# Kernel optimization log

Hardware: AMD Instinct MI355X
Metric: run time of the kernel (lower is better)

## Reference

```python
import jax, jax.numpy as jnp
import numpy as np

LAYER_LAYOUT = [64, 128, 128, 128, 10]
B, D, D_OUT, L_GNN = 16, 128, 10, 3
N = sum(LAYER_LAYOUT)            # 458 nodes per graph


def _build_edge_index():
    # nn_to_edge_index: fully-connected bipartite edges between consecutive layers
    offs = np.cumsum([0] + LAYER_LAYOUT)
    src, dst = [], []
    for i in range(1, len(LAYER_LAYOUT)):
        s = np.arange(offs[i - 1], offs[i])
        d = np.arange(offs[i], offs[i + 1])
        ss, dd = np.meshgrid(s, d, indexing='ij')
        src.append(ss.ravel())
        dst.append(dd.ravel())
    return np.stack([np.concatenate(src), np.concatenate(dst)])  # [2, E]


def setup_inputs() -> dict:
    key = jax.random.key(0)
    ks = jax.random.split(key, 8)
    E = 42240
    edge_index = jnp.asarray(_build_edge_index(), dtype=jnp.int64)
    return {
        'node_features': jax.random.normal(ks[0], (B, N, D), jnp.float32),
        'edge_attr': jax.random.normal(ks[1], (B, E, D), jnp.float32),
        'w_msg': jax.random.normal(ks[2], (L_GNN, 3 * D, D), jnp.float32) / jnp.sqrt(3.0 * D),
        'b_msg': jnp.zeros((L_GNN, D), jnp.float32),
        'w_self': jax.random.normal(ks[3], (L_GNN, D, D), jnp.float32) / jnp.sqrt(1.0 * D),
        'b_self': jnp.zeros((L_GNN, D), jnp.float32),
        'w1': jax.random.normal(ks[4], (D, D), jnp.float32) / jnp.sqrt(1.0 * D),
        'b1': jnp.zeros((D,), jnp.float32),
        'w2': jax.random.normal(ks[5], (D, D), jnp.float32) / jnp.sqrt(1.0 * D),
        'b2': jnp.zeros((D,), jnp.float32),
        'w3': jax.random.normal(ks[6], (D, D_OUT), jnp.float32) / jnp.sqrt(1.0 * D),
        'b3': jnp.zeros((D_OUT,), jnp.float32),
        'edge_index': edge_index,
    }


def reference(node_features, edge_attr, w_msg, b_msg, w_self, b_self,
              w1, b1, w2, b2, w3, b3, edge_index):
    src, dst = edge_index[0], edge_index[1]
    E = src.shape[0]
    # in-degree per destination node (shared across the batch)
    deg = jax.ops.segment_sum(jnp.ones((E,), node_features.dtype), dst, num_segments=N)
    denom = jnp.maximum(deg, 1.0)[:, None]  # [N, 1]

    def aggregate(m):  # m: [B, E, D] -> [B, N, D] mean over incoming edges
        return jax.vmap(lambda mm: jax.ops.segment_sum(mm, dst, num_segments=N))(m) / denom

    x = node_features
    for l in range(L_GNN):
        # edge message: relu(W [x_src, x_dst, e])
        m = jnp.concatenate([x[:, src], x[:, dst], edge_attr], axis=-1)  # [B, E, 3D]
        m = jax.nn.relu(jnp.einsum('bef,fd->bed', m, w_msg[l]) + b_msg[l])
        agg = aggregate(m)  # [B, N, D]
        x = jax.nn.relu(jnp.einsum('bnf,fd->bnd', x, w_self[l]) + b_self[l] + agg)

    # graph_features == 'mean' over nodes, then proj_out MLP head
    g = x.mean(axis=1)  # [B, D]
    h = jax.nn.relu(g @ w1 + b1)
    h = jax.nn.relu(h @ w2 + b2)
    return h @ w3 + b3  # [B, D_OUT]
```

## Files before the change

### kernel.cpp

```cpp
#include <hip/hip_runtime.h>
#include <hip/hip_bf16.h>

#define D 128
#define NNODES 458
#define BATCH 16
#define ETOT 42240
#define LGNN 3
#define SPLITS 8

typedef __bf16 bf16x8 __attribute__((ext_vector_type(8)));
typedef float f32x4 __attribute__((ext_vector_type(4)));

__device__ inline bf16x8 cvt8v(f32x4 a, f32x4 b) {
    bf16x8 r;
    r[0] = (__bf16)a[0]; r[1] = (__bf16)a[1]; r[2] = (__bf16)a[2]; r[3] = (__bf16)a[3];
    r[4] = (__bf16)b[0]; r[5] = (__bf16)b[1]; r[6] = (__bf16)b[2]; r[7] = (__bf16)b[3];
    return r;
}

__global__ __launch_bounds__(256) void cvt_edge_kernel(
    const f32x4* __restrict__ src, bf16x8* __restrict__ dst)
{
    const size_t total = (size_t)BATCH * ETOT * (D / 8);
    size_t i = (size_t)blockIdx.x * 256 + threadIdx.x;
    const size_t stride = (size_t)gridDim.x * 256;
    for (; i < total; i += stride) {
        f32x4 a = __builtin_nontemporal_load(&src[2 * i]);
        f32x4 b = __builtin_nontemporal_load(&src[2 * i + 1]);
        dst[i] = cvt8v(a, b);
    }
}

__global__ __launch_bounds__(256) void node_proj_kernel(
    const float* __restrict__ x,
    const float* __restrict__ wmsg_l,
    const float* __restrict__ bmsg_l,
    const float* __restrict__ wself_l,
    const float* __restrict__ bself_l,
    float* __restrict__ asrc, float* __restrict__ bdst, float* __restrict__ xs,
    float* __restrict__ agg)
{
    const int b     = blockIdx.y;
    const int n0    = blockIdx.x * 16;
    const int which = blockIdx.z;
    const int tid   = threadIdx.x;

    __shared__ float xt[16 * D];
    for (int i = tid; i < 16 * D; i += 256) {
        int r = i >> 7;
        int n = n0 + r; if (n >= NNODES) n = NNODES - 1;
        xt[i] = x[((size_t)b * NNODES + n) * D + (i & 127)];
    }
    __syncthreads();

    const int d    = tid & 127;
    const int half = tid >> 7;

    const float* w = (which == 0) ? wmsg_l
                   : (which == 1) ? (wmsg_l + D * D)
                                  : wself_l;

    float acc[8] = {};
    for (int k = 0; k < D; ++k) {
        float wv = w[k * D + d];
#pragma unroll
        for (int r = 0; r < 8; ++r)
            acc[r] += xt[(half * 8 + r) * D + k] * wv;
    }

    const float bias = (which == 1) ? bmsg_l[d] : (which == 2) ? bself_l[d] : 0.f;
    float* outp = (which == 0) ? asrc : (which == 1) ? bdst : xs;
#pragma unroll
    for (int r = 0; r < 8; ++r) {
        int n = n0 + half * 8 + r;
        if (n < NNODES) {
            size_t o = ((size_t)b * NNODES + n) * D + d;
            outp[o] = acc[r] + bias;
            if (which == 0) agg[o] = 0.f;
        }
    }
}

__global__ __launch_bounds__(256) void edge_kernel(
    const bf16x8* __restrict__ eb,
    const float* __restrict__ w3,
    const float* __restrict__ asrc,
    const float* __restrict__ bdst,
    float* __restrict__ agg)
{
    const int tile  = blockIdx.x;
    const int b     = blockIdx.y;
    const int split = blockIdx.z;

    int j0, Nsrc, Ndst, e_off, src_off, dst_off;
    if (tile < 8)       { j0 = tile * 16;        Nsrc = 64;  Ndst = 128; e_off = 0;     src_off = 0;   dst_off = 64;  }
    else if (tile < 16) { j0 = (tile - 8) * 16;  Nsrc = 128; Ndst = 128; e_off = 8192;  src_off = 64;  dst_off = 192; }
    else if (tile < 24) { j0 = (tile - 16) * 16; Nsrc = 128; Ndst = 128; e_off = 24576; src_off = 192; dst_off = 320; }
    else                { j0 = 0;                Nsrc = 128; Ndst = 10;  e_off = 40960; src_off = 320; dst_off = 448; }

    const int chunk = Nsrc / SPLITS;
    const int s0    = split * chunk;

    const int tid  = threadIdx.x;
    const int wave = tid >> 6;
    const int lane = tid & 63;
    const int lm   = lane & 15;
    const int q    = lane >> 4;

    bf16x8 bfrag[2][4];
#pragma unroll
    for (int t = 0; t < 2; ++t) {
        int n = wave * 32 + t * 16 + lm;
#pragma unroll
        for (int kk = 0; kk < 4; ++kk)
#pragma unroll
            for (int j = 0; j < 8; ++j)
                bfrag[t][kk][j] = (__bf16)w3[(kk * 32 + q * 8 + j) * D + n];
    }

    float bpv[2][4];
#pragma unroll
    for (int t = 0; t < 2; ++t)
#pragma unroll
        for (int r = 0; r < 4; ++r) {
            int j = j0 + q * 4 + r; if (j > Ndst - 1) j = Ndst - 1;
            bpv[t][r] = bdst[((size_t)b * NNODES + dst_off + j) * D + wave * 32 + t * 16 + lm];
        }

    int m_eff = (j0 + lm < Ndst) ? lm : (Ndst - 1 - j0);
    const bf16x8* ap = eb +
        ((size_t)b * ETOT + e_off + (size_t)s0 * Ndst + j0 + m_eff) * 16 + q;
    const float* as_ptr = asrc + ((size_t)b * NNODES + src_off + s0) * D;

    float acc[2][4] = {};
#pragma unroll 4
    for (int s = 0; s < chunk; ++s) {
        bf16x8 afrag[4];
#pragma unroll
        for (int kk = 0; kk < 4; ++kk) afrag[kk] = ap[kk * 4];
        float as0 = as_ptr[wave * 32 + lm];
        float as1 = as_ptr[wave * 32 + 16 + lm];
        ap += Ndst * 16;
        as_ptr += D;

#pragma unroll
        for (int t = 0; t < 2; ++t) {
            f32x4 c = {0.f, 0.f, 0.f, 0.f};
#pragma unroll
            for (int kk = 0; kk < 4; ++kk)
                c = __builtin_amdgcn_mfma_f32_16x16x32_bf16(afrag[kk], bfrag[t][kk], c, 0, 0, 0);
            float as_d = t ? as1 : as0;
#pragma unroll
            for (int r = 0; r < 4; ++r) {
                float v = c[r] + as_d + bpv[t][r];
                acc[t][r] += fmaxf(v, 0.f);
            }
        }
    }

    const float inv_deg = 1.0f / (float)Nsrc;
#pragma unroll
    for (int t = 0; t < 2; ++t)
#pragma unroll
        for (int r = 0; r < 4; ++r) {
            int j = j0 + q * 4 + r;
            if (j < Ndst)
                atomicAdd(&agg[((size_t)b * NNODES + dst_off + j) * D + wave * 32 + t * 16 + lm],
                          acc[t][r] * inv_deg);
        }
}

__global__ __launch_bounds__(256) void update_kernel(
    const float4* __restrict__ xs, const float4* __restrict__ agg,
    float4* __restrict__ x)
{
    int i = blockIdx.x * 256 + threadIdx.x;
    int rowi = i >> 5;
    int n = rowi % NNODES;
    float4 v = xs[i];
    if (n >= 64) {
        float4 a = agg[i];
        v.x += a.x; v.y += a.y; v.z += a.z; v.w += a.w;
    }
    v.x = fmaxf(v.x, 0.f); v.y = fmaxf(v.y, 0.f);
    v.z = fmaxf(v.z, 0.f); v.w = fmaxf(v.w, 0.f);
    x[i] = v;
}

__global__ __launch_bounds__(256) void head_kernel(
    const float* __restrict__ x,
    const float* __restrict__ w1, const float* __restrict__ b1,
    const float* __restrict__ w2, const float* __restrict__ b2,
    const float* __restrict__ w3, const float* __restrict__ b3,
    float* __restrict__ out)
{
    const int b = blockIdx.x;
    const int tid = threadIdx.x;
    __shared__ float tmp[256];
    __shared__ float g[128], h1[128], h2[128];

    const int d = tid & 127, half = tid >> 7;
    float s = 0.f;
    for (int n = half; n < NNODES; n += 2)
        s += x[((size_t)b * NNODES + n) * D + d];
    tmp[tid] = s;
    __syncthreads();
    if (tid < 128) g[tid] = (tmp[tid] + tmp[tid + 128]) * (1.0f / (float)NNODES);
    __syncthreads();

    if (tid < 128) {
        float a = 0.f;
        for (int k = 0; k < D; ++k) a += g[k] * w1[k * D + tid];
        h1[tid] = fmaxf(a + b1[tid], 0.f);
    }
    __syncthreads();
    if (tid < 128) {
        float a = 0.f;
        for (int k = 0; k < D; ++k) a += h1[k] * w2[k * D + tid];
        h2[tid] = fmaxf(a + b2[tid], 0.f);
    }
    __syncthreads();
    if (tid < 10) {
        float a = 0.f;
        for (int k = 0; k < D; ++k) a += h2[k] * w3[k * 10 + tid];
        out[b * 10 + tid] = a + b3[tid];
    }
}

extern "C" void kernel_launch(void* const* d_in, const int* in_sizes, int n_in,
                              void* d_out, int out_size, void* d_ws, size_t ws_size,
                              hipStream_t stream) {
    const float* node_features = (const float*)d_in[0];
    const float* edge_attr     = (const float*)d_in[1];
    const float* w_msg         = (const float*)d_in[2];
    const float* b_msg         = (const float*)d_in[3];
    const float* w_self        = (const float*)d_in[4];
    const float* b_self        = (const float*)d_in[5];
    const float* w1 = (const float*)d_in[6];
    const float* b1 = (const float*)d_in[7];
    const float* w2 = (const float*)d_in[8];
    const float* b2 = (const float*)d_in[9];
    const float* w3 = (const float*)d_in[10];
    const float* b3 = (const float*)d_in[11];
    float* out = (float*)d_out;

    float* ws = (float*)d_ws;
    const size_t SZ = (size_t)BATCH * NNODES * D;
    float* x_ws = ws;
    float* asrc = ws + SZ;
    float* bdst = ws + 2 * SZ;
    float* xs   = ws + 3 * SZ;
    float* agg  = ws + 4 * SZ;
    bf16x8* eb  = (bf16x8*)(ws + 5 * SZ);

    cvt_edge_kernel<<<dim3(2048), 256, 0, stream>>>(
        (const f32x4*)edge_attr, eb);

    for (int l = 0; l < LGNN; ++l) {
        const float* xin    = (l == 0) ? node_features : x_ws;
        const float* wmsg_l = w_msg + (size_t)l * 384 * 128;
        node_proj_kernel<<<dim3(29, 16, 3), 256, 0, stream>>>(
            xin, wmsg_l, b_msg + l * 128, w_self + (size_t)l * 128 * 128,
            b_self + l * 128, asrc, bdst, xs, agg);
        edge_kernel<<<dim3(25, 16, SPLITS), 256, 0, stream>>>(
            eb, wmsg_l + 256 * 128, asrc, bdst, agg);
        update_kernel<<<dim3(916), 256, 0, stream>>>(
            (const float4*)xs, (const float4*)agg, (float4*)x_ws);
    }
    head_kernel<<<dim3(16), 256, 0, stream>>>(x_ws, w1, b1, w2, b2, w3, b3, out);
}
```

Measured before the change: 914.1 us.

## Fuse node update into projections, merge prep work, pre-transpose bf16 message weights

The per-layer update kernel is removed: the next layer's projection and the head kernel now apply relu(xs + agg) while loading. The three projection GEMMs (source, destination and self) are computed in one block, so the node tile is read once instead of three times. Edge conversion, a bf16 transpose of the edge-message weights and the layer-0 projection are merged into a single prep launch. The edge kernel can then load its weight fragments as vector bf16 reads instead of strided scalar float loads. This cuts launches and intermediate traffic, at the cost of more registers in the projection and xs/agg being updated in place.

```diff
diff --git a/kernel.cpp b/kernel.cpp
--- a/kernel.cpp
+++ b/kernel.cpp
@@ -18,72 +18,122 @@
     return r;
 }
 
-__global__ __launch_bounds__(256) void cvt_edge_kernel(
-    const f32x4* __restrict__ src, bf16x8* __restrict__ dst)
-{
-    const size_t total = (size_t)BATCH * ETOT * (D / 8);
-    size_t i = (size_t)blockIdx.x * 256 + threadIdx.x;
-    const size_t stride = (size_t)gridDim.x * 256;
-    for (; i < total; i += stride) {
-        f32x4 a = __builtin_nontemporal_load(&src[2 * i]);
-        f32x4 b = __builtin_nontemporal_load(&src[2 * i + 1]);
-        dst[i] = cvt8v(a, b);
-    }
-}
-
-__global__ __launch_bounds__(256) void node_proj_kernel(
-    const float* __restrict__ x,
-    const float* __restrict__ wmsg_l,
-    const float* __restrict__ bmsg_l,
-    const float* __restrict__ wself_l,
-    const float* __restrict__ bself_l,
-    float* __restrict__ asrc, float* __restrict__ bdst, float* __restrict__ xs,
-    float* __restrict__ agg)
-{
-    const int b     = blockIdx.y;
-    const int n0    = blockIdx.x * 16;
-    const int which = blockIdx.z;
-    const int tid   = threadIdx.x;
-
-    __shared__ float xt[16 * D];
-    for (int i = tid; i < 16 * D; i += 256) {
-        int r = i >> 7;
+__device__ __forceinline__ void proj_body(
+    int b, int n0, int mode,
+    const float* xsrc,
+    const float* aggin,
+    const float* __restrict__ wmsg_l, const float* __restrict__ bmsg_l,
+    const float* __restrict__ wself_l, const float* __restrict__ bself_l,
+    float* __restrict__ asrc, float* __restrict__ bdst,
+    float* xs_out, float* __restrict__ agg, float* xt)
+{
+    const int tid = threadIdx.x;
+    for (int i4 = tid; i4 < 512; i4 += 256) {
+        int r = i4 >> 5;
         int n = n0 + r; if (n >= NNODES) n = NNODES - 1;
-        xt[i] = x[((size_t)b * NNODES + n) * D + (i & 127)];
-    }
-    __syncthreads();
-
-    const int d    = tid & 127;
-    const int half = tid >> 7;
-
-    const float* w = (which == 0) ? wmsg_l
-                   : (which == 1) ? (wmsg_l + D * D)
-                                  : wself_l;
-
-    float acc[8] = {};
-    for (int k = 0; k < D; ++k) {
-        float wv = w[k * D + d];
-#pragma unroll
-        for (int r = 0; r < 8; ++r)
-            acc[r] += xt[(half * 8 + r) * D + k] * wv;
-    }
-
-    const float bias = (which == 1) ? bmsg_l[d] : (which == 2) ? bself_l[d] : 0.f;
-    float* outp = (which == 0) ? asrc : (which == 1) ? bdst : xs;
+        size_t o = ((size_t)b * NNODES + n) * 32 + (i4 & 31);
+        float4 v = ((const float4*)xsrc)[o];
+        if (mode) {
+            if (n >= 64) {
+                float4 a = ((const float4*)aggin)[o];
+                v.x += a.x; v.y += a.y; v.z += a.z; v.w += a.w;
+            }
+            v.x = fmaxf(v.x, 0.f); v.y = fmaxf(v.y, 0.f);
+            v.z = fmaxf(v.z, 0.f); v.w = fmaxf(v.w, 0.f);
+        }
+        ((float4*)xt)[i4] = v;
+    }
+    __syncthreads();
+
+    const int d = tid & 127, half = tid >> 7;
+    float acc0[8] = {}, acc1[8] = {}, acc2[8] = {};
+    const float4* xt4 = (const float4*)xt;
+    for (int k4 = 0; k4 < 32; ++k4) {
+        float4 xv[8];
+#pragma unroll
+        for (int r = 0; r < 8; ++r) xv[r] = xt4[(half * 8 + r) * 32 + k4];
+#pragma unroll
+        for (int i = 0; i < 4; ++i) {
+            int k = k4 * 4 + i;
+            float w1v = wmsg_l[k * D + d];
+            float w2v = wmsg_l[(D + k) * D + d];
+            float wsv = wself_l[k * D + d];
+#pragma unroll
+            for (int r = 0; r < 8; ++r) {
+                float xe = (i == 0) ? xv[r].x : (i == 1) ? xv[r].y
+                         : (i == 2) ? xv[r].z : xv[r].w;
+                acc0[r] += xe * w1v;
+                acc1[r] += xe * w2v;
+                acc2[r] += xe * wsv;
+            }
+        }
+    }
+    const float bm = bmsg_l[d], bs = bself_l[d];
 #pragma unroll
     for (int r = 0; r < 8; ++r) {
         int n = n0 + half * 8 + r;
         if (n < NNODES) {
             size_t o = ((size_t)b * NNODES + n) * D + d;
-            outp[o] = acc[r] + bias;
-            if (which == 0) agg[o] = 0.f;
-        }
-    }
+            asrc[o]   = acc0[r];
+            bdst[o]   = acc1[r] + bm;
+            xs_out[o] = acc2[r] + bs;
+            agg[o]    = 0.f;
+        }
+    }
+}
+
+__global__ __launch_bounds__(256) void prep_kernel(
+    const f32x4* __restrict__ edge_attr, bf16x8* __restrict__ eb,
+    const float* __restrict__ w_msg, __bf16* __restrict__ wT,
+    const float* __restrict__ node_features,
+    const float* __restrict__ bmsg0,
+    const float* __restrict__ wself0, const float* __restrict__ bself0,
+    float* __restrict__ asrc, float* __restrict__ bdst,
+    float* __restrict__ xs, float* __restrict__ agg)
+{
+    __shared__ float xt[16 * D];
+    const int bid = blockIdx.x;
+    const int tid = threadIdx.x;
+    if (bid < 2048) {
+        const size_t total = (size_t)BATCH * ETOT * (D / 8);
+        size_t i = (size_t)bid * 256 + tid;
+        const size_t stride = (size_t)2048 * 256;
+        for (; i < total; i += stride) {
+            f32x4 a = __builtin_nontemporal_load(&edge_attr[2 * i]);
+            f32x4 b = __builtin_nontemporal_load(&edge_attr[2 * i + 1]);
+            eb[i] = cvt8v(a, b);
+        }
+    } else if (bid < 2051) {
+        const int l = bid - 2048;
+        const float* w3s = w_msg + (size_t)l * 384 * 128 + 256 * 128;
+        __bf16* wTl = wT + (size_t)l * 128 * 128;
+        for (int idx = tid; idx < 128 * 128; idx += 256) {
+            int n = idx >> 7, k = idx & 127;
+            wTl[idx] = (__bf16)w3s[k * 128 + n];
+        }
+    } else {
+        const int bid2 = bid - 2051;
+        const int bx = bid2 % 29, b = bid2 / 29;
+        proj_body(b, bx * 16, 0, node_features, nullptr,
+                  w_msg, bmsg0, wself0, bself0, asrc, bdst, xs, agg, xt);
+    }
+}
+
+__global__ __launch_bounds__(256) void node_proj_kernel(
+    const float* xs_in, const float* __restrict__ agg_in,
+    const float* __restrict__ wmsg_l, const float* __restrict__ bmsg_l,
+    const float* __restrict__ wself_l, const float* __restrict__ bself_l,
+    float* __restrict__ asrc, float* __restrict__ bdst,
+    float* xs, float* __restrict__ agg)
+{
+    __shared__ float xt[16 * D];
+    proj_body(blockIdx.y, blockIdx.x * 16, 1, xs_in, agg_in,
+              wmsg_l, bmsg_l, wself_l, bself_l, asrc, bdst, xs, agg, xt);
 }
 
 __global__ __launch_bounds__(256) void edge_kernel(
     const bf16x8* __restrict__ eb,
-    const float* __restrict__ w3,
+    const __bf16* __restrict__ wT_l,
     const float* __restrict__ asrc,
     const float* __restrict__ bdst,
     float* __restrict__ agg)
@@ -113,9 +163,7 @@
         int n = wave * 32 + t * 16 + lm;
 #pragma unroll
         for (int kk = 0; kk < 4; ++kk)
-#pragma unroll
-            for (int j = 0; j < 8; ++j)
-                bfrag[t][kk][j] = (__bf16)w3[(kk * 32 + q * 8 + j) * D + n];
+            bfrag[t][kk] = *(const bf16x8*)(wT_l + n * 128 + kk * 32 + q * 8);
     }
 
     float bpv[2][4];
@@ -170,25 +218,8 @@
         }
 }
 
-__global__ __launch_bounds__(256) void update_kernel(
-    const float4* __restrict__ xs, const float4* __restrict__ agg,
-    float4* __restrict__ x)
-{
-    int i = blockIdx.x * 256 + threadIdx.x;
-    int rowi = i >> 5;
-    int n = rowi % NNODES;
-    float4 v = xs[i];
-    if (n >= 64) {
-        float4 a = agg[i];
-        v.x += a.x; v.y += a.y; v.z += a.z; v.w += a.w;
-    }
-    v.x = fmaxf(v.x, 0.f); v.y = fmaxf(v.y, 0.f);
-    v.z = fmaxf(v.z, 0.f); v.w = fmaxf(v.w, 0.f);
-    x[i] = v;
-}
-
 __global__ __launch_bounds__(256) void head_kernel(
-    const float* __restrict__ x,
+    const float* __restrict__ xs, const float* __restrict__ agg,
     const float* __restrict__ w1, const float* __restrict__ b1,
     const float* __restrict__ w2, const float* __restrict__ b2,
     const float* __restrict__ w3, const float* __restrict__ b3,
@@ -201,8 +232,12 @@
 
     const int d = tid & 127, half = tid >> 7;
     float s = 0.f;
-    for (int n = half; n < NNODES; n += 2)
-        s += x[((size_t)b * NNODES + n) * D + d];
+    for (int n = half; n < NNODES; n += 2) {
+        size_t o = ((size_t)b * NNODES + n) * D + d;
+        float v = xs[o];
+        if (n >= 64) v += agg[o];
+        s += fmaxf(v, 0.f);
+    }
     tmp[tid] = s;
     __syncthreads();
     if (tid < 128) g[tid] = (tmp[tid] + tmp[tid + 128]) * (1.0f / (float)NNODES);
@@ -246,26 +281,28 @@
 
     float* ws = (float*)d_ws;
     const size_t SZ = (size_t)BATCH * NNODES * D;
-    float* x_ws = ws;
-    float* asrc = ws + SZ;
-    float* bdst = ws + 2 * SZ;
-    float* xs   = ws + 3 * SZ;
-    float* agg  = ws + 4 * SZ;
-    bf16x8* eb  = (bf16x8*)(ws + 5 * SZ);
-
-    cvt_edge_kernel<<<dim3(2048), 256, 0, stream>>>(
-        (const f32x4*)edge_attr, eb);
+    float* asrc = ws;
+    float* bdst = ws + SZ;
+    float* xs   = ws + 2 * SZ;
+    float* agg  = ws + 3 * SZ;
+    bf16x8* eb  = (bf16x8*)(ws + 4 * SZ);
+    __bf16* wT  = (__bf16*)(ws + 4 * SZ + (size_t)BATCH * ETOT * (D / 2));
+
+    prep_kernel<<<dim3(2048 + 3 + 464), 256, 0, stream>>>(
+        (const f32x4*)edge_attr, eb, w_msg, wT, node_features,
+        b_msg, w_self, b_self, asrc, bdst, xs, agg);
 
     for (int l = 0; l < LGNN; ++l) {
-        const float* xin    = (l == 0) ? node_features : x_ws;
-        const float* wmsg_l = w_msg + (size_t)l * 384 * 128;
-        node_proj_kernel<<<dim3(29, 16, 3), 256, 0, stream>>>(
-            xin, wmsg_l, b_msg + l * 128, w_self + (size_t)l * 128 * 128,
-            b_self + l * 128, asrc, bdst, xs, agg);
+        if (l > 0) {
+            const float* wmsg_l = w_msg + (size_t)l * 384 * 128;
+            node_proj_kernel<<<dim3(29, 16), 256, 0, stream>>>(
+                xs, agg, wmsg_l, b_msg + l * 128,
+                w_self + (size_t)l * 128 * 128, b_self + l * 128,
+                asrc, bdst, xs, agg);
+        }
         edge_kernel<<<dim3(25, 16, SPLITS), 256, 0, stream>>>(
-            eb, wmsg_l + 256 * 128, asrc, bdst, agg);
-        update_kernel<<<dim3(916), 256, 0, stream>>>(
-            (const float4*)xs, (const float4*)agg, (float4*)x_ws);
-    }
-    head_kernel<<<dim3(16), 256, 0, stream>>>(x_ws, w1, b1, w2, b2, w3, b3, out);
-}
+            eb, wT + (size_t)l * 128 * 128, asrc, bdst, agg);
+    }
+    head_kernel<<<dim3(16), 256, 0, stream>>>(
+        xs, agg, w1, b1, w2, b2, w3, b3, out);
+}
```

New measurement: 3.105 ms. 3.4x slower.

## Replace edge-kernel atomics with two split partial buffers and pre-transposed bf16 weights

Applied to the files above, without the earlier changes.

The edge kernel's source dimension is now split into 2 chunks instead of 8. Each split writes its partial aggregate to its own buffer with plain stores rather than atomicAdd, so node_proj no longer zeroes agg. The update kernel sums the two partial buffers. A one-time kernel also transposes and converts the edge-message weight slice to bf16, so each block loads its B fragments with vector loads instead of 32 strided scalar loads. The trade-off is fewer blocks in the edge grid (800 instead of 3200) with a longer serial loop per block, plus one extra partial buffer to read in the update kernel.

```diff
diff --git a/kernel.cpp b/kernel.cpp
--- a/kernel.cpp
+++ b/kernel.cpp
@@ -6,7 +6,7 @@
 #define BATCH 16
 #define ETOT 42240
 #define LGNN 3
-#define SPLITS 8
+#define ESPLITS 2
 
 typedef __bf16 bf16x8 __attribute__((ext_vector_type(8)));
 typedef float f32x4 __attribute__((ext_vector_type(4)));
@@ -31,14 +31,25 @@
     }
 }
 
+__global__ __launch_bounds__(256) void wt_kernel(
+    const float* __restrict__ w_msg, __bf16* __restrict__ wT)
+{
+    const int l = blockIdx.x;
+    const float* w3s = w_msg + (size_t)l * 384 * 128 + 256 * 128;
+    __bf16* wTl = wT + (size_t)l * 128 * 128;
+    for (int idx = threadIdx.x; idx < 128 * 128; idx += 256) {
+        int n = idx >> 7, k = idx & 127;
+        wTl[idx] = (__bf16)w3s[k * 128 + n];
+    }
+}
+
 __global__ __launch_bounds__(256) void node_proj_kernel(
     const float* __restrict__ x,
     const float* __restrict__ wmsg_l,
     const float* __restrict__ bmsg_l,
     const float* __restrict__ wself_l,
     const float* __restrict__ bself_l,
-    float* __restrict__ asrc, float* __restrict__ bdst, float* __restrict__ xs,
-    float* __restrict__ agg)
+    float* __restrict__ asrc, float* __restrict__ bdst, float* __restrict__ xs)
 {
     const int b     = blockIdx.y;
     const int n0    = blockIdx.x * 16;
@@ -76,17 +87,16 @@
         if (n < NNODES) {
             size_t o = ((size_t)b * NNODES + n) * D + d;
             outp[o] = acc[r] + bias;
-            if (which == 0) agg[o] = 0.f;
         }
     }
 }
 
 __global__ __launch_bounds__(256) void edge_kernel(
     const bf16x8* __restrict__ eb,
-    const float* __restrict__ w3,
+    const __bf16* __restrict__ wT_l,
     const float* __restrict__ asrc,
     const float* __restrict__ bdst,
-    float* __restrict__ agg)
+    float* __restrict__ aggp)
 {
     const int tile  = blockIdx.x;
     const int b     = blockIdx.y;
@@ -98,7 +108,7 @@
     else if (tile < 24) { j0 = (tile - 16) * 16; Nsrc = 128; Ndst = 128; e_off = 24576; src_off = 192; dst_off = 320; }
     else                { j0 = 0;                Nsrc = 128; Ndst = 10;  e_off = 40960; src_off = 320; dst_off = 448; }
 
-    const int chunk = Nsrc / SPLITS;
+    const int chunk = Nsrc / ESPLITS;
     const int s0    = split * chunk;
 
     const int tid  = threadIdx.x;
@@ -113,9 +123,7 @@
         int n = wave * 32 + t * 16 + lm;
 #pragma unroll
         for (int kk = 0; kk < 4; ++kk)
-#pragma unroll
-            for (int j = 0; j < 8; ++j)
-                bfrag[t][kk][j] = (__bf16)w3[(kk * 32 + q * 8 + j) * D + n];
+            bfrag[t][kk] = *(const bf16x8*)(wT_l + n * 128 + kk * 32 + q * 8);
     }
 
     float bpv[2][4];
@@ -159,19 +167,21 @@
     }
 
     const float inv_deg = 1.0f / (float)Nsrc;
+    float* aout = aggp + (size_t)split * BATCH * NNODES * D;
 #pragma unroll
     for (int t = 0; t < 2; ++t)
 #pragma unroll
         for (int r = 0; r < 4; ++r) {
             int j = j0 + q * 4 + r;
             if (j < Ndst)
-                atomicAdd(&agg[((size_t)b * NNODES + dst_off + j) * D + wave * 32 + t * 16 + lm],
-                          acc[t][r] * inv_deg);
+                aout[((size_t)b * NNODES + dst_off + j) * D + wave * 32 + t * 16 + lm] =
+                    acc[t][r] * inv_deg;
         }
 }
 
 __global__ __launch_bounds__(256) void update_kernel(
-    const float4* __restrict__ xs, const float4* __restrict__ agg,
+    const float4* __restrict__ xs,
+    const float4* __restrict__ agg0, const float4* __restrict__ agg1,
     float4* __restrict__ x)
 {
     int i = blockIdx.x * 256 + threadIdx.x;
@@ -179,8 +189,8 @@
     int n = rowi % NNODES;
     float4 v = xs[i];
     if (n >= 64) {
-        float4 a = agg[i];
-        v.x += a.x; v.y += a.y; v.z += a.z; v.w += a.w;
+        float4 a = agg0[i], c = agg1[i];
+        v.x += a.x + c.x; v.y += a.y + c.y; v.z += a.z + c.z; v.w += a.w + c.w;
     }
     v.x = fmaxf(v.x, 0.f); v.y = fmaxf(v.y, 0.f);
     v.z = fmaxf(v.z, 0.f); v.w = fmaxf(v.w, 0.f);
@@ -250,22 +260,24 @@
     float* asrc = ws + SZ;
     float* bdst = ws + 2 * SZ;
     float* xs   = ws + 3 * SZ;
-    float* agg  = ws + 4 * SZ;
-    bf16x8* eb  = (bf16x8*)(ws + 5 * SZ);
-
-    cvt_edge_kernel<<<dim3(2048), 256, 0, stream>>>(
-        (const f32x4*)edge_attr, eb);
+    float* aggp = ws + 4 * SZ;
+    bf16x8* eb  = (bf16x8*)(ws + 6 * SZ);
+    __bf16* wT  = (__bf16*)(ws + 6 * SZ + (size_t)BATCH * ETOT * (D / 2));
+
+    cvt_edge_kernel<<<dim3(2048), 256, 0, stream>>>((const f32x4*)edge_attr, eb);
+    wt_kernel<<<dim3(3), 256, 0, stream>>>(w_msg, wT);
 
     for (int l = 0; l < LGNN; ++l) {
         const float* xin    = (l == 0) ? node_features : x_ws;
         const float* wmsg_l = w_msg + (size_t)l * 384 * 128;
         node_proj_kernel<<<dim3(29, 16, 3), 256, 0, stream>>>(
             xin, wmsg_l, b_msg + l * 128, w_self + (size_t)l * 128 * 128,
-            b_self + l * 128, asrc, bdst, xs, agg);
-        edge_kernel<<<dim3(25, 16, SPLITS), 256, 0, stream>>>(
-            eb, wmsg_l + 256 * 128, asrc, bdst, agg);
+            b_self + l * 128, asrc, bdst, xs);
+        edge_kernel<<<dim3(25, 16, ESPLITS), 256, 0, stream>>>(
+            eb, wT + (size_t)l * 128 * 128, asrc, bdst, aggp);
         update_kernel<<<dim3(916), 256, 0, stream>>>(
-            (const float4*)xs, (const float4*)agg, (float4*)x_ws);
+            (const float4*)xs, (const float4*)aggp,
+            (const float4*)(aggp + SZ), (float4*)x_ws);
     }
     head_kernel<<<dim3(16), 256, 0, stream>>>(x_ws, w1, b1, w2, b2, w3, b3, out);
 }
```

New measurement: 971.0 us. +6.2%, slower.
